# Optimization experiments

Measured on AMD Instinct MI355X. Metric: run time of the kernel, lower is better.

The kernel has to match this reference:

```python
import jax, jax.numpy as jnp
import numpy as np

B, A, T, H, E, O, TY, SC, AG = 8, 64, 12, 128, 128, 128, 8, 32, 16


def setup_inputs() -> dict:
    ks = jax.random.split(jax.random.key(0), 32)

    def rn(k, shape, s=1.0):
        return jax.random.normal(k, shape, dtype=jnp.float32) * s

    z = lambda *s: jnp.zeros(s, dtype=jnp.float32)
    return {
        "trajectories": rn(ks[0], (B, A, T, 3)),
        "normalized_trajectories": rn(ks[1], (B, A, T, 3)),
        "agent_type": rn(ks[2], (B, A, TY)),
        "scene_data": rn(ks[3], (B, T, SC)),
        "agent_data": rn(ks[4], (B, A, T, AG)),
        "relevant_agents": jnp.ones((B, A), dtype=jnp.float32),
        "W_in": rn(ks[5], (6, H), 0.05), "b_in": z(H),
        "W_node_type": rn(ks[6], (TY, H), 0.05), "b_node_type": z(H),
        "W_agent": rn(ks[7], (AG, H), 0.05), "b_agent": z(H),
        "W_scene": rn(ks[8], (SC, H), 0.05), "b_scene": z(H),
        "W_edge_in": rn(ks[9], (2 * 6 + 2 * TY, E), 0.05), "b_edge_in": z(E),
        "W_edge_type": rn(ks[10], (2 * TY, E), 0.05), "b_edge_type": z(E),
        "W_edge": rn(ks[11], (2 * H + E, E), 0.05), "b_edge": z(E),
        "W_self": rn(ks[12], (H + E + TY, E), 0.05), "b_self": z(E),
        "W_e2n": rn(ks[13], (E, H), 0.05), "b_e2n": z(H),
        "W_ih": rn(ks[14], (5 * H, 4 * H), 0.05),
        "W_hh": rn(ks[15], (H, 4 * H), 0.05),
        "b_ih": z(4 * H), "b_hh": z(4 * H),
        "W_pred": rn(ks[16], (H, O), 0.05), "b_pred": z(O),
    }


def reference(trajectories, normalized_trajectories, agent_type, scene_data, agent_data,
              relevant_agents, W_in, b_in, W_node_type, b_node_type, W_agent, b_agent,
              W_scene, b_scene, W_edge_in, b_edge_in, W_edge_type, b_edge_type,
              W_edge, b_edge, W_self, b_self, W_e2n, b_e2n,
              W_ih, W_hh, b_ih, b_hh, W_pred, b_pred):
    # cat(normalized, raw) along last dim -> 2*(input_dim+1)=6
    both = jnp.concatenate([normalized_trajectories, trajectories], axis=-1)  # [B,A,T,6]
    coord = jax.nn.relu(both @ W_in + b_in)                                   # [B,A,T,H]
    type_enc = agent_type @ W_node_type + b_node_type                          # [B,A,H]
    agent_enc = (agent_data @ W_agent + b_agent) * relevant_agents[:, :, None, None]  # [B,A,T,H]
    scene_enc = scene_data @ W_scene + b_scene                                 # [B,T,H]

    b, a, t_steps = both.shape[0], both.shape[1], both.shape[2]
    Hd = W_in.shape[1]
    Ed = W_edge.shape[1]
    ty = agent_type.shape[-1]

    # initial pairwise edge states from agent features at t=0 + type-pair encoding
    ty_i = jnp.broadcast_to(agent_type[:, :, None, :], (b, a, a, ty))
    ty_j = jnp.broadcast_to(agent_type[:, None, :, :], (b, a, a, ty))
    ty_pair = jnp.concatenate([ty_i, ty_j], axis=-1)                           # [B,A,A,2*TY]
    f0 = both[:, :, 0, :]                                                      # [B,A,6]
    f_i = jnp.broadcast_to(f0[:, :, None, :], (b, a, a, f0.shape[-1]))
    f_j = jnp.broadcast_to(f0[:, None, :, :], (b, a, a, f0.shape[-1]))
    edge0 = (jnp.concatenate([f_i, f_j, ty_pair], axis=-1) @ W_edge_in + b_edge_in
             + ty_pair @ W_edge_type + b_edge_type)                            # [B,A,A,E]

    h0 = jnp.zeros((b, a, Hd), both.dtype)
    c0 = jnp.zeros((b, a, Hd), both.dtype)
    se0 = jnp.zeros((b, a, Ed), both.dtype)

    def step(carry, xs):
        h, c, es, se = carry
        coord_t, scene_t, agent_t, t = xs
        # edge MLP on gathered node pairs (BN is identity in eval, dropout off)
        hi = jnp.broadcast_to(h[:, :, None, :], (b, a, a, Hd))
        hj = jnp.broadcast_to(h[:, None, :, :], (b, a, a, Hd))
        es_new = jnp.concatenate([hi, hj, es], axis=-1) @ W_edge + b_edge      # [B,A,A,E]
        se_new = jnp.concatenate([h, se, agent_type], axis=-1) @ W_self + b_self  # [B,A,E]
        agg = es_new.sum(axis=2) + se_new                                      # scatter-sum to nodes
        node_edges = (agg @ W_e2n + b_e2n) * (t > 0).astype(h.dtype)           # zeros at t==0
        x = jnp.concatenate(
            [coord_t, type_enc, node_edges,
             jnp.broadcast_to(scene_t[:, None, :], (b, a, Hd)), agent_t], axis=-1)  # [B,A,5H]
        gates = x @ W_ih + h @ W_hh + b_ih + b_hh
        gi, gf, gg, go = jnp.split(gates, 4, axis=-1)
        c_new = jax.nn.sigmoid(gf) * c + jax.nn.sigmoid(gi) * jnp.tanh(gg)
        h_new = jax.nn.sigmoid(go) * jnp.tanh(c_new)
        out = jax.nn.relu(h_new @ W_pred + b_pred)                             # layer_pred
        return (h_new, c_new, es_new, se_new), out

    xs = (jnp.moveaxis(coord, 2, 0), jnp.moveaxis(scene_enc, 1, 0),
          jnp.moveaxis(agent_enc, 2, 0), jnp.arange(t_steps))
    _, ys = jax.lax.scan(step, (h0, c0, edge0, se0), xs)                       # ys: [T,B,A,O]
    return jnp.moveaxis(ys, 0, 2)                                              # [B,A,T,O]
```

## Files before the change

kernel.cpp:

```cpp
#include <hip/hip_runtime.h>

constexpr int NB = 8, NA = 64, NT = 12, NH = 128, NTY = 8, NSC = 32, NAG = 16;

struct Params {
    const float *traj, *ntraj, *ty, *sd, *adata, *rel;
    const float *W_in, *b_in, *W_nt, *b_nt, *W_ag, *b_ag, *W_sc, *b_sc;
    const float *W_ein, *b_ein, *W_ety, *b_ety;
    const float *W_edge, *b_edge, *W_self, *b_self, *W_e2n, *b_e2n;
    const float *W_ih, *W_hh, *b_ih, *b_hh, *W_pred, *b_pred;
    float *h0, *h1, *c, *se, *R;
    float *Wty, *Wsc, *Wag, *Wcomb, *vbase, *vag, *vbe, *sesty, *Xs, *out;
};

__global__ __launch_bounds__(512) void k_prelude(Params p) {
    const int blk = blockIdx.x, tid = threadIdx.x;
    if (blk < 185) {
        const int c = tid;
        __shared__ float lrow[NH];
        __shared__ float b1[NH], b2[NH], b3[NH], b4[NH];
        if (blk < 184) {
            const float* src; int ihoff, row; float* dst;
            if (blk < 8)       { row = blk;      src = p.W_nt  + row * NH; ihoff = 128; dst = p.Wty; }
            else if (blk < 40) { row = blk - 8;  src = p.W_sc  + row * NH; ihoff = 384; dst = p.Wsc; }
            else if (blk < 56) { row = blk - 40; src = p.W_ag  + row * NH; ihoff = 512; dst = p.Wag; }
            else               { row = blk - 56; src = p.W_e2n + row * NH; ihoff = 256; dst = p.Wcomb; }
            if (c < NH) lrow[c] = src[c];
            __syncthreads();
            float acc = 0.f;
            for (int k = 0; k < NH; ++k) acc += lrow[k] * p.W_ih[(ihoff + k) * 512 + c];
            dst[row * 512 + c] = acc;
        } else {
            if (c < NH) { b1[c] = p.b_nt[c]; b2[c] = p.b_sc[c]; b3[c] = p.b_ag[c]; b4[c] = p.b_e2n[c]; }
            __syncthreads();
            float vb = p.b_ih[c] + p.b_hh[c], va = 0.f, ve = 0.f;
            for (int k = 0; k < NH; ++k) {
                vb += b1[k] * p.W_ih[(128 + k) * 512 + c] + b2[k] * p.W_ih[(384 + k) * 512 + c];
                va += b3[k] * p.W_ih[(512 + k) * 512 + c];
                ve += b4[k] * p.W_ih[(256 + k) * 512 + c];
            }
            p.vbase[c] = vb; p.vag[c] = va; p.vbe[c] = ve;
        }
    } else {
        const int r0g = (blk - 185) * 4;
        const int b = r0g >> 6;
        const int q = tid >> 7, n = tid & 127;
        const int row = r0g + q, i = row & 63;
        __shared__ float lf[NA][6];
        __shared__ float lt[NA][NTY];
        __shared__ float sumf[6], sumt[NTY];
        if (tid < NA) {
            int j = tid, rj = b * NA + j;
            for (int k = 0; k < 3; ++k) {
                lf[j][k]     = p.ntraj[(rj * NT + 0) * 3 + k];
                lf[j][3 + k] = p.traj [(rj * NT + 0) * 3 + k];
            }
            for (int k = 0; k < NTY; ++k) lt[j][k] = p.ty[rj * NTY + k];
        }
        p.h0[row * NH + n] = 0.f;
        p.c [row * NH + n] = 0.f;
        p.se[row * NH + n] = 0.f;
        __syncthreads();
        if (tid < 6) {
            float s = 0.f; for (int j = 0; j < NA; ++j) s += lf[j][tid];
            sumf[tid] = s;
        } else if (tid < 6 + NTY) {
            int k = tid - 6; float s = 0.f;
            for (int j = 0; j < NA; ++j) s += lt[j][k];
            sumt[k] = s;
        }
        __syncthreads();
        float acc_i = p.b_ein[n] + p.b_ety[n];
        for (int k = 0; k < 6; ++k)   acc_i += lf[i][k] * p.W_ein[k * NH + n];
        for (int k = 0; k < NTY; ++k) acc_i += lt[i][k] * (p.W_ein[(12 + k) * NH + n] + p.W_ety[k * NH + n]);
        float acc_j = 0.f;
        for (int k = 0; k < 6; ++k)   acc_j += sumf[k] * p.W_ein[(6 + k) * NH + n];
        for (int k = 0; k < NTY; ++k) acc_j += sumt[k] * (p.W_ein[(20 + k) * NH + n] + p.W_ety[(NTY + k) * NH + n]);
        p.R[row * NH + n] = 64.f * acc_i + acc_j;
        float sv = p.b_self[n];
        for (int k = 0; k < NTY; ++k) sv += lt[i][k] * p.W_self[(2 * NH + k) * NH + n];
        p.sesty[row * NH + n] = sv;
    }
}

__global__ __launch_bounds__(512) void k_xstatic(Params p) {
    const int g = blockIdx.x, tid = threadIdx.x, b = g >> 6;
    __shared__ float coordL[NT][NH];
    __shared__ float sceneL[NT][NSC];
    __shared__ float agentL[NT][NAG];
    __shared__ float tyL[NTY];
    const float relv = p.rel[g];
    for (int idx = tid; idx < NT * NH; idx += 512) {
        int r = idx >> 7, k = idx & 127;
        float acc = p.b_in[k];
        const float* nt = p.ntraj + (g * NT + r) * 3;
        const float* tr = p.traj  + (g * NT + r) * 3;
        for (int j = 0; j < 3; ++j) acc += nt[j] * p.W_in[j * NH + k] + tr[j] * p.W_in[(3 + j) * NH + k];
        coordL[r][k] = fmaxf(acc, 0.f);
    }
    for (int i = tid; i < NT * NSC; i += 512) { int r = i >> 5, k = i & 31; sceneL[r][k] = p.sd[(b * NT + r) * NSC + k]; }
    for (int i = tid; i < NT * NAG; i += 512) { int r = i >> 4, k = i & 15; agentL[r][k] = p.adata[(g * NT + r) * NAG + k] * relv; }
    if (tid < NTY) tyL[tid] = p.ty[g * NTY + tid];
    __syncthreads();
    const int c = tid;
    float base = p.vbase[c] + relv * p.vag[c];
    for (int i = 0; i < NTY; ++i) base += tyL[i] * p.Wty[i * 512 + c];
    const float vbeL = p.vbe[c];
    float acc[NT];
#pragma unroll
    for (int r = 0; r < NT; ++r) acc[r] = base + (r > 0 ? vbeL : 0.f);
    for (int k = 0; k < NH; ++k) { float w = p.W_ih[k * 512 + c];
#pragma unroll
        for (int r = 0; r < NT; ++r) acc[r] += coordL[r][k] * w; }
    for (int k = 0; k < NSC; ++k) { float w = p.Wsc[k * 512 + c];
#pragma unroll
        for (int r = 0; r < NT; ++r) acc[r] += sceneL[r][k] * w; }
    for (int k = 0; k < NAG; ++k) { float w = p.Wag[k * 512 + c];
#pragma unroll
        for (int r = 0; r < NT; ++r) acc[r] += agentL[r][k] * w; }
#pragma unroll
    for (int r = 0; r < NT; ++r) p.Xs[((size_t)(g * NT + r)) * 512 + c] = acc[r];
}

__global__ __launch_bounds__(1024) void k_step(Params p, int t) {
    const int tid = threadIdx.x;
    const int r0 = blockIdx.x * 2;
    const int b = r0 >> 6;
    const int n = tid & 127;
    const int g8 = tid >> 7;
    const float* __restrict__ hcur = (t & 1) ? p.h1 : p.h0;
    float* hnxt = (t & 1) ? p.h0 : p.h1;

    __shared__ float lh[2][NH], lR[2][NH], lse[2][NH];
    __shared__ float psum[8][NH];
    __shared__ float ps2[8][NH];
    __shared__ __align__(16) float psA[4][8][2][NH];
    __shared__ float psO[8][NH];
    __shared__ float lagg[2][NH];
    __shared__ __align__(16) float lgp[8][2][512];

    if (t == NT) {
        if (tid < 256) lh[tid >> 7][tid & 127] = hcur[(r0 + (tid >> 7)) * NH + (tid & 127)];
        __syncthreads();
        {
            const int r = g8 & 1, kq = g8 >> 1;
            float s = 0.f;
            const float* wp = p.W_pred + n;
#pragma unroll
            for (int k = 32 * kq; k < 32 * kq + 32; ++k) s += lh[r][k] * wp[k * NH];
            psO[g8][n] = s;
        }
        __syncthreads();
        if (tid < 256) {
            const int rr = tid >> 7, k = tid & 127;
            float v = psO[rr][k] + psO[2 + rr][k] + psO[4 + rr][k] + psO[6 + rr][k] + p.b_pred[k];
            p.out[((size_t)(r0 + rr) * NT + (NT - 1)) * NH + k] = fmaxf(v, 0.f);
        }
        return;
    }

    if (tid < 256) {
        int rr = tid >> 7, k = tid & 127;
        lh[rr][k]  = hcur[(r0 + rr) * NH + k];
        lR[rr][k]  = p.R [(r0 + rr) * NH + k];
        lse[rr][k] = p.se[(r0 + rr) * NH + k];
    }
    if (t > 0) {
        float s = 0.f;
        const float* hb = hcur + (b * NA + g8 * 8) * NH + n;
#pragma unroll
        for (int j = 0; j < 8; ++j) s += hb[j * NH];
        psum[g8][n] = s;
    }
    __syncthreads();

    {
        const int pa  = tid >> 8;
        const int kq  = (tid >> 5) & 7;
        const int t32 = tid & 31;
        const float* wb = (pa == 0) ? p.W_edge
                        : (pa == 1) ? p.W_edge + 2 * NH * NH
                        : (pa == 2) ? p.W_self
                                    : p.W_self + NH * NH;
        const float* d0 = (pa == 1) ? lR[0] : (pa == 3) ? lse[0] : lh[0];
        const float* d1 = (pa == 1) ? lR[1] : (pa == 3) ? lse[1] : lh[1];
        const float4* wv = (const float4*)wb;
        float4 a0 = {0.f, 0.f, 0.f, 0.f}, a1 = {0.f, 0.f, 0.f, 0.f};
#pragma unroll
        for (int k = 16 * kq; k < 16 * kq + 16; ++k) {
            float4 w4 = wv[k * 32 + t32];
            float x0 = d0[k], x1 = d1[k];
            a0.x += x0 * w4.x; a0.y += x0 * w4.y; a0.z += x0 * w4.z; a0.w += x0 * w4.w;
            a1.x += x1 * w4.x; a1.y += x1 * w4.y; a1.z += x1 * w4.z; a1.w += x1 * w4.w;
        }
        *(float4*)&psA[pa][kq][0][4 * t32] = a0;
        *(float4*)&psA[pa][kq][1][4 * t32] = a1;
    }
    if (t > 0) {
        float s = 0.f;
        const float* w2 = p.W_edge + NH * NH + n;
#pragma unroll
        for (int k = 16 * g8; k < 16 * g8 + 16; ++k) {
            float hv = psum[0][k] + psum[1][k] + psum[2][k] + psum[3][k]
                     + psum[4][k] + psum[5][k] + psum[6][k] + psum[7][k];
            s += hv * w2[k * NH];
        }
        ps2[g8][n] = s;
    }
    if (t > 0) {
        const int r = g8 & 1, kq = g8 >> 1;
        float s = 0.f;
        const float* wp = p.W_pred + n;
#pragma unroll
        for (int k = 32 * kq; k < 32 * kq + 32; ++k) s += lh[r][k] * wp[k * NH];
        psO[g8][n] = s;
    }
    __syncthreads();

    if (tid < 256) {
        int rr = tid >> 7, k = tid & 127;
        float shw2v = 0.f;
        if (t > 0) {
#pragma unroll
            for (int q = 0; q < 8; ++q) shw2v += ps2[q][k];
        }
        float a1v = 0.f, a3v = 0.f, aSv = 0.f;
#pragma unroll
        for (int kq = 0; kq < 8; ++kq) {
            a1v += psA[0][kq][rr][k];
            a3v += psA[1][kq][rr][k];
            aSv += psA[2][kq][rr][k] + psA[3][kq][rr][k];
        }
        float Rn = 64.f * a1v + shw2v + a3v + 64.f * p.b_edge[k];
        float Sn = aSv + p.sesty[(r0 + rr) * NH + k];
        p.R [(r0 + rr) * NH + k] = Rn;
        p.se[(r0 + rr) * NH + k] = Sn;
        lagg[rr][k] = Rn + Sn;
    } else if (tid >= 512 && tid < 768 && t > 0) {
        const int rc = tid - 512, rr = rc >> 7, k = rc & 127;
        float v = psO[rr][k] + psO[2 + rr][k] + psO[4 + rr][k] + psO[6 + rr][k] + p.b_pred[k];
        p.out[((size_t)(r0 + rr) * NT + (t - 1)) * NH + k] = fmaxf(v, 0.f);
    }
    __syncthreads();

    {
        const int kq = tid >> 7;
        const int cq = tid & 127;
        float4 a0 = {0.f, 0.f, 0.f, 0.f}, a1 = {0.f, 0.f, 0.f, 0.f};
        if (kq == 0) {
            a0 = *(const float4*)&p.Xs[((size_t)r0 * NT + t) * 512 + 4 * cq];
            a1 = *(const float4*)&p.Xs[((size_t)(r0 + 1) * NT + t) * 512 + 4 * cq];
        }
        if (t > 0) {
            const float4* wc = (const float4*)p.Wcomb;
            const float4* wh = (const float4*)p.W_hh;
#pragma unroll
            for (int k = 16 * kq; k < 16 * kq + 16; ++k) {
                float4 w4 = wc[k * 128 + cq];
                float g0 = lagg[0][k], g1 = lagg[1][k];
                a0.x += g0 * w4.x; a0.y += g0 * w4.y; a0.z += g0 * w4.z; a0.w += g0 * w4.w;
                a1.x += g1 * w4.x; a1.y += g1 * w4.y; a1.z += g1 * w4.z; a1.w += g1 * w4.w;
            }
#pragma unroll
            for (int k = 16 * kq; k < 16 * kq + 16; ++k) {
                float4 w4 = wh[k * 128 + cq];
                float h0v = lh[0][k], h1v = lh[1][k];
                a0.x += h0v * w4.x; a0.y += h0v * w4.y; a0.z += h0v * w4.z; a0.w += h0v * w4.w;
                a1.x += h1v * w4.x; a1.y += h1v * w4.y; a1.z += h1v * w4.z; a1.w += h1v * w4.w;
            }
        }
        *(float4*)&lgp[kq][0][4 * cq] = a0;
        *(float4*)&lgp[kq][1][4 * cq] = a1;
    }
    __syncthreads();

    if (tid < 256) {
        const int rr = tid >> 7, k = tid & 127, g = r0 + rr;
        float gi = 0.f, gf = 0.f, gg = 0.f, go = 0.f;
#pragma unroll
        for (int kq = 0; kq < 8; ++kq) {
            gi += lgp[kq][rr][k];
            gf += lgp[kq][rr][NH + k];
            gg += lgp[kq][rr][2 * NH + k];
            go += lgp[kq][rr][3 * NH + k];
        }
        float si = 1.f / (1.f + expf(-gi));
        float sf = 1.f / (1.f + expf(-gf));
        float so = 1.f / (1.f + expf(-go));
        float cn = sf * p.c[g * NH + k] + si * tanhf(gg);
        float hn = so * tanhf(cn);
        p.c[g * NH + k] = cn;
        hnxt[g * NH + k] = hn;
    }
}

extern "C" void kernel_launch(void* const* d_in, const int* in_sizes, int n_in,
                              void* d_out, int out_size, void* d_ws, size_t ws_size,
                              hipStream_t stream) {
    const float* const* in = (const float* const*)d_in;
    Params p;
    p.traj = in[0]; p.ntraj = in[1]; p.ty = in[2]; p.sd = in[3]; p.adata = in[4]; p.rel = in[5];
    p.W_in = in[6]; p.b_in = in[7]; p.W_nt = in[8]; p.b_nt = in[9];
    p.W_ag = in[10]; p.b_ag = in[11]; p.W_sc = in[12]; p.b_sc = in[13];
    p.W_ein = in[14]; p.b_ein = in[15]; p.W_ety = in[16]; p.b_ety = in[17];
    p.W_edge = in[18]; p.b_edge = in[19]; p.W_self = in[20]; p.b_self = in[21];
    p.W_e2n = in[22]; p.b_e2n = in[23];
    p.W_ih = in[24]; p.W_hh = in[25]; p.b_ih = in[26]; p.b_hh = in[27];
    p.W_pred = in[28]; p.b_pred = in[29];

    float* ws = (float*)d_ws;
    const size_t S = (size_t)NB * NA * NH;
    p.h0 = ws;
    p.h1 = ws + S;
    p.c  = ws + 2 * S;
    p.se = ws + 3 * S;
    p.R  = ws + 4 * S;
    float* w = ws + 5 * S;
    p.Wty   = w;              w += 8 * 512;
    p.Wsc   = w;              w += 32 * 512;
    p.Wag   = w;              w += 16 * 512;
    p.Wcomb = w;              w += 128 * 512;
    p.vbase = w;              w += 512;
    p.vag   = w;              w += 512;
    p.vbe   = w;              w += 512;
    p.sesty = w;              w += (size_t)NB * NA * NH;
    p.Xs    = w;              w += (size_t)NB * NA * NT * 512;
    p.out = (float*)d_out;

    k_prelude<<<313, 512, 0, stream>>>(p);
    k_xstatic<<<NB * NA, 512, 0, stream>>>(p);
    for (int t = 0; t < NT; ++t)
        k_step<<<NB * NA / 2, 1024, 0, stream>>>(p, t);
    k_step<<<NB * NA / 2, 1024, 0, stream>>>(p, NT);
}
```

Baseline: 189.9 us.

## Fold step t=0 into xstatic and final prediction into last step kernel

The t=0 LSTM step, which has zero hidden state and zero edge inputs, is now computed inside k_xstatic. That kernel also initialises c, h1, se and the updated R. The final output projection moves into the tail of the t=NT-1 step kernel, so two of the fourteen k_step launches are removed. This cuts launch overhead and serialisation gaps between kernels, in exchange for extra work and synchronisation in xstatic and the last step.

```diff
diff --git a/kernel.cpp b/kernel.cpp
--- a/kernel.cpp
+++ b/kernel.cpp
@@ -57,8 +57,6 @@
             for (int k = 0; k < NTY; ++k) lt[j][k] = p.ty[rj * NTY + k];
         }
         p.h0[row * NH + n] = 0.f;
-        p.c [row * NH + n] = 0.f;
-        p.se[row * NH + n] = 0.f;
         __syncthreads();
         if (tid < 6) {
             float s = 0.f; for (int j = 0; j < NA; ++j) s += lf[j][tid];
@@ -88,6 +86,9 @@
     __shared__ float sceneL[NT][NSC];
     __shared__ float agentL[NT][NAG];
     __shared__ float tyL[NTY];
+    __shared__ float lg0[512];
+    __shared__ float R0L[NH];
+    __shared__ float psR[4][NH];
     const float relv = p.rel[g];
     for (int idx = tid; idx < NT * NH; idx += 512) {
         int r = idx >> 7, k = idx & 127;
@@ -100,6 +101,7 @@
     for (int i = tid; i < NT * NSC; i += 512) { int r = i >> 5, k = i & 31; sceneL[r][k] = p.sd[(b * NT + r) * NSC + k]; }
     for (int i = tid; i < NT * NAG; i += 512) { int r = i >> 4, k = i & 15; agentL[r][k] = p.adata[(g * NT + r) * NAG + k] * relv; }
     if (tid < NTY) tyL[tid] = p.ty[g * NTY + tid];
+    if (tid >= 512 - NH) R0L[tid - (512 - NH)] = p.R[g * NH + (tid - (512 - NH))];
     __syncthreads();
     const int c = tid;
     float base = p.vbase[c] + relv * p.vag[c];
@@ -118,7 +120,29 @@
 #pragma unroll
         for (int r = 0; r < NT; ++r) acc[r] += agentL[r][k] * w; }
 #pragma unroll
-    for (int r = 0; r < NT; ++r) p.Xs[((size_t)(g * NT + r)) * 512 + c] = acc[r];
+    for (int r = 1; r < NT; ++r) p.Xs[((size_t)(g * NT + r)) * 512 + c] = acc[r];
+    lg0[c] = acc[0];
+    {
+        const int kq = tid >> 7, n2 = tid & 127;
+        float s = 0.f;
+        const float* w3 = p.W_edge + 2 * NH * NH + n2;
+#pragma unroll 8
+        for (int k = 32 * kq; k < 32 * kq + 32; ++k) s += R0L[k] * w3[k * NH];
+        psR[kq][n2] = s;
+    }
+    __syncthreads();
+    if (tid < NH) {
+        const int n = tid;
+        float gi = lg0[n], gg = lg0[2 * NH + n], go = lg0[3 * NH + n];
+        float si = 1.f / (1.f + expf(-gi));
+        float so = 1.f / (1.f + expf(-go));
+        float cn = si * tanhf(gg);
+        float hn = so * tanhf(cn);
+        p.c [g * NH + n] = cn;
+        p.h1[g * NH + n] = hn;
+        p.se[g * NH + n] = p.sesty[g * NH + n];
+        p.R [g * NH + n] = psR[0][n] + psR[1][n] + psR[2][n] + psR[3][n] + 64.f * p.b_edge[n];
+    }
 }
 
 __global__ __launch_bounds__(1024) void k_step(Params p, int t) {
@@ -138,33 +162,13 @@
     __shared__ float lagg[2][NH];
     __shared__ __align__(16) float lgp[8][2][512];
 
-    if (t == NT) {
-        if (tid < 256) lh[tid >> 7][tid & 127] = hcur[(r0 + (tid >> 7)) * NH + (tid & 127)];
-        __syncthreads();
-        {
-            const int r = g8 & 1, kq = g8 >> 1;
-            float s = 0.f;
-            const float* wp = p.W_pred + n;
-#pragma unroll
-            for (int k = 32 * kq; k < 32 * kq + 32; ++k) s += lh[r][k] * wp[k * NH];
-            psO[g8][n] = s;
-        }
-        __syncthreads();
-        if (tid < 256) {
-            const int rr = tid >> 7, k = tid & 127;
-            float v = psO[rr][k] + psO[2 + rr][k] + psO[4 + rr][k] + psO[6 + rr][k] + p.b_pred[k];
-            p.out[((size_t)(r0 + rr) * NT + (NT - 1)) * NH + k] = fmaxf(v, 0.f);
-        }
-        return;
-    }
-
     if (tid < 256) {
         int rr = tid >> 7, k = tid & 127;
         lh[rr][k]  = hcur[(r0 + rr) * NH + k];
         lR[rr][k]  = p.R [(r0 + rr) * NH + k];
         lse[rr][k] = p.se[(r0 + rr) * NH + k];
     }
-    if (t > 0) {
+    {
         float s = 0.f;
         const float* hb = hcur + (b * NA + g8 * 8) * NH + n;
 #pragma unroll
@@ -195,7 +199,7 @@
         *(float4*)&psA[pa][kq][0][4 * t32] = a0;
         *(float4*)&psA[pa][kq][1][4 * t32] = a1;
     }
-    if (t > 0) {
+    {
         float s = 0.f;
         const float* w2 = p.W_edge + NH * NH + n;
 #pragma unroll
@@ -206,7 +210,7 @@
         }
         ps2[g8][n] = s;
     }
-    if (t > 0) {
+    {
         const int r = g8 & 1, kq = g8 >> 1;
         float s = 0.f;
         const float* wp = p.W_pred + n;
@@ -219,10 +223,8 @@
     if (tid < 256) {
         int rr = tid >> 7, k = tid & 127;
         float shw2v = 0.f;
-        if (t > 0) {
-#pragma unroll
-            for (int q = 0; q < 8; ++q) shw2v += ps2[q][k];
-        }
+#pragma unroll
+        for (int q = 0; q < 8; ++q) shw2v += ps2[q][k];
         float a1v = 0.f, a3v = 0.f, aSv = 0.f;
 #pragma unroll
         for (int kq = 0; kq < 8; ++kq) {
@@ -235,7 +237,7 @@
         p.R [(r0 + rr) * NH + k] = Rn;
         p.se[(r0 + rr) * NH + k] = Sn;
         lagg[rr][k] = Rn + Sn;
-    } else if (tid >= 512 && tid < 768 && t > 0) {
+    } else if (tid >= 512 && tid < 768) {
         const int rc = tid - 512, rr = rc >> 7, k = rc & 127;
         float v = psO[rr][k] + psO[2 + rr][k] + psO[4 + rr][k] + psO[6 + rr][k] + p.b_pred[k];
         p.out[((size_t)(r0 + rr) * NT + (t - 1)) * NH + k] = fmaxf(v, 0.f);
@@ -250,7 +252,7 @@
             a0 = *(const float4*)&p.Xs[((size_t)r0 * NT + t) * 512 + 4 * cq];
             a1 = *(const float4*)&p.Xs[((size_t)(r0 + 1) * NT + t) * 512 + 4 * cq];
         }
-        if (t > 0) {
+        {
             const float4* wc = (const float4*)p.Wcomb;
             const float4* wh = (const float4*)p.W_hh;
 #pragma unroll
@@ -290,6 +292,25 @@
         float hn = so * tanhf(cn);
         p.c[g * NH + k] = cn;
         hnxt[g * NH + k] = hn;
+        lh[rr][k] = hn;
+    }
+
+    if (t == NT - 1) {
+        __syncthreads();
+        {
+            const int r = g8 & 1, kq = g8 >> 1;
+            float s = 0.f;
+            const float* wp = p.W_pred + n;
+#pragma unroll
+            for (int k = 32 * kq; k < 32 * kq + 32; ++k) s += lh[r][k] * wp[k * NH];
+            psO[g8][n] = s;
+        }
+        __syncthreads();
+        if (tid < 256) {
+            const int rr = tid >> 7, k = tid & 127;
+            float v = psO[rr][k] + psO[2 + rr][k] + psO[4 + rr][k] + psO[6 + rr][k] + p.b_pred[k];
+            p.out[((size_t)(r0 + rr) * NT + (NT - 1)) * NH + k] = fmaxf(v, 0.f);
+        }
     }
 }
 
@@ -328,7 +349,6 @@
 
     k_prelude<<<313, 512, 0, stream>>>(p);
     k_xstatic<<<NB * NA, 512, 0, stream>>>(p);
-    for (int t = 0; t < NT; ++t)
+    for (int t = 1; t < NT; ++t)
         k_step<<<NB * NA / 2, 1024, 0, stream>>>(p, t);
-    k_step<<<NB * NA / 2, 1024, 0, stream>>>(p, NT);
 }
```

After: 281.9 us. 1.48x slower.
